# Kernel optimization log

Measured on AMD Instinct MI355X. Metric: run time of the kernel, lower is better.

The kernel has to match this reference:

```python
import jax, jax.numpy as jnp
import numpy as np

V = 23
C_IN = 256
C_OUT = 256
N = 16384
BN_EPS = 1e-5


def _make_shift(c, sign):
    # shift_in:  idx[i*c+j] = (i*c + j + j*c) % (c*V)
    # shift_out: idx[i*c+j] = (i*c + j - j*c) % (c*V)
    i = np.arange(V)[:, None]
    j = np.arange(c)[None, :]
    idx = (i * c + j + sign * j * c) % (c * V)
    return jnp.asarray(idx.reshape(-1), dtype=jnp.int32)


def setup_inputs() -> dict:
    key = jax.random.key(0)
    k1, k2, k3 = jax.random.split(key, 3)
    x0 = jax.random.normal(k1, (N, C_IN, V), dtype=jnp.float32)
    # Linear_weight ~ N(0, sqrt(1/out_channels))
    W = jax.random.normal(k2, (C_IN, C_OUT), dtype=jnp.float32) * np.sqrt(1.0 / C_OUT)
    bias = jnp.zeros((1, 1, C_OUT), dtype=jnp.float32)
    # Feature_Mask param (init 0 in original; randomized for a non-trivial baseline)
    mask = jax.random.normal(k3, (1, V, C_IN), dtype=jnp.float32) * 0.1
    bn_weight = jnp.ones((V * C_OUT,), dtype=jnp.float32)
    bn_bias = jnp.zeros((V * C_OUT,), dtype=jnp.float32)
    shift_in = _make_shift(C_IN, +1)
    shift_out = _make_shift(C_OUT, -1)
    return {"x0": x0, "W": W, "bias": bias, "mask": mask,
            "bn_weight": bn_weight, "bn_bias": bn_bias,
            "shift_in": shift_in, "shift_out": shift_out}


def reference(x0, W, bias, mask, bn_weight, bn_bias, shift_in, shift_out):
    n, c, v = x0.shape
    c_out = W.shape[1]
    # (n, c, v) -> (n, v*c), channel-shift gather
    x = jnp.transpose(x0, (0, 2, 1)).reshape(n, v * c)
    x = x[:, shift_in]                       # gather along feature dim
    x = x.reshape(n, v, c)
    x = x * (jnp.tanh(mask) + 1.0)           # learned soft mask
    x = jnp.einsum('nwc,cd->nwd', x, W) + bias
    x = x.reshape(n, v * c_out)
    x = x[:, shift_out]                      # shift-back gather
    # BatchNorm1d over v*c_out features, training-mode batch stats (biased var)
    mean = jnp.mean(x, axis=0)
    var = jnp.var(x, axis=0)
    x = (x - mean) * jax.lax.rsqrt(var + BN_EPS) * bn_weight + bn_bias
    x = x.reshape(n, v, c_out).transpose(0, 2, 1)
    # in_channels == out_channels -> down is identity
    x = x + x0
    return jax.nn.relu(x)
```

## Files before the change

kernel.cpp:

```cpp
#include <hip/hip_runtime.h>
#include <hip/hip_bf16.h>

#define NV 23
#define NTOT 16384
#define FLAT (NV * 256)
#define FLAT4 (FLAT / 4)
#define CH 184
#define NS 3
#define SLAB 23552

#define NB0 64
#define ROFF0 32768
#define NB1 64
#define ROFF1 32768
#define OOFF1 103424

#define NPART 256
#define WT8_OFF 248832
#define TAB8_OFF 314368
#define PSUM_OFF 337920
#define PSSQ_OFF (PSUM_OFF + NPART * FLAT * 4)
#define WS_NEED (PSSQ_OFF + NPART * FLAT * 4)

typedef short s16x8 __attribute__((ext_vector_type(8)));
typedef float f32x4 __attribute__((ext_vector_type(4)));
typedef unsigned u32x4 __attribute__((ext_vector_type(4)));
typedef long long i64t;

__device__ __forceinline__ int divNV(int x) { return (int)(((unsigned)x * 45591u) >> 20); }
__device__ __forceinline__ unsigned f2bf(float f) {
  unsigned u = __float_as_uint(f);
  u += 0x7fffu + ((u >> 16) & 1u);
  return u >> 16;
}
__device__ __forceinline__ int fsw(int w) { return ((w + (w >> 3)) * 3) & 7; }

__device__ __forceinline__ void gl_lds16(const void* g, void* l) {
  __builtin_amdgcn_global_load_lds(
      (const __attribute__((address_space(1))) unsigned*)(unsigned long long)(uintptr_t)g,
      (__attribute__((address_space(3))) unsigned*)(unsigned)(uintptr_t)l, 16, 0, 0);
}

__global__ void k_prep(const float* __restrict__ W, const float* __restrict__ mask,
                       short* __restrict__ Wt, char* __restrict__ Wt8,
                       unsigned* __restrict__ tab, unsigned* __restrict__ tab8,
                       float* __restrict__ sums) {
  int idx = blockIdx.x * 256 + threadIdx.x;
  int d = idx >> 8, c = idx & 255;
  float wv = W[c * 256 + d];
  Wt[idx] = (short)f2bf(wv);
  Wt8[idx] = (char)__builtin_amdgcn_cvt_pk_fp8_f32(wv, wv, 0, false);
  if (idx < FLAT) {
    int cc = divNV(idx);
    int v = idx - NV * cc;
    int cm = cc - NV * divNV(cc);
    int w = v - cm; w += (w >> 31) & NV;
    unsigned m2b = f2bf(tanhf(mask[(w << 8) + cc]) + 1.0f) << 16;
    tab[idx]  = m2b | (unsigned)((w << 9) + ((cc << 1) ^ (fsw(w) << 4)));
    tab8[idx] = m2b | (unsigned)((w << 8) + (cc ^ (fsw(w) << 4)));
  }
  if (idx < 2 * FLAT) sums[idx] = 0.0f;
}

__global__ void k_finalize(const float* __restrict__ sum, const float* __restrict__ ssq,
                           const float* __restrict__ psum, const float* __restrict__ pssq,
                           const float* __restrict__ bnw, const float* __restrict__ bnb,
                           float* __restrict__ An2, float* __restrict__ Bn2) {
  __shared__ float red[2][4][64];
  const int t = threadIdx.x;
  const int f0 = blockIdx.x * 64;
  if (psum) {
    const int fl = t & 63, c = t >> 6;
    float S = 0.f, Q = 0.f;
    for (int b = 0; b < 64; ++b) {
      S += psum[(size_t)(c * 64 + b) * FLAT + f0 + fl];
      Q += pssq[(size_t)(c * 64 + b) * FLAT + f0 + fl];
    }
    red[0][c][fl] = S;
    red[1][c][fl] = Q;
    __syncthreads();
  }
  if (t < 64) {
    int idx = f0 + t;
    float S, Q;
    if (psum) {
      S = red[0][0][t] + red[0][1][t] + red[0][2][t] + red[0][3][t];
      Q = red[1][0][t] + red[1][1][t] + red[1][2][t] + red[1][3][t];
    } else {
      S = sum[idx]; Q = ssq[idx];
    }
    int w = idx >> 8, d = idx & 255;
    float mean = S * (1.0f / NTOT);
    float var  = Q * (1.0f / NTOT) - mean * mean;
    float inv  = rsqrtf(var + 1e-5f);
    int i = w + d; i -= NV * divNV(i);
    float a = inv * bnw[i * 256 + d];
    An2[d * NV + i] = a;
    Bn2[d * NV + i] = bnb[i * 256 + d] - mean * a;
  }
}

__global__ __launch_bounds__(512) void k_stats(
    const float* __restrict__ x0, const char* __restrict__ Wt8,
    const unsigned* __restrict__ tab8, float* __restrict__ sum, float* __restrict__ ssq,
    float* __restrict__ psum, float* __restrict__ pssq) {
  __shared__ char smem[126976];

  const int tid = threadIdx.x;
  const int lane = tid & 63;
  const int wv = tid >> 6;
  const int l15 = lane & 15;
  const int lg = lane >> 4;
  const int d0 = wv * 32;
  const int ch0 = wv * CH;
  const int fr0 = fsw(l15) << 4;
  const int fr1 = fsw(16 + l15) << 4;

  i64t bfr8[2][8];
#pragma unroll
  for (int nt = 0; nt < 2; ++nt)
#pragma unroll
    for (int kt = 0; kt < 8; ++kt)
      bfr8[nt][kt] = *(const i64t*)(Wt8 + (d0 + nt * 16 + l15) * 256 + kt * 32 + lg * 8);

  u32x4 tbr[NS];
#pragma unroll
  for (int s = 0; s < NS; ++s)
    if (s * 64 + lane < CH) tbr[s] = *(const u32x4*)(tab8 + 4 * (ch0 + s * 64 + lane));

  for (int i = tid; i < 2304; i += 512) {
    int b = i / 576;
    *(int*)(smem + b * 8192 + 5888 + (i - b * 576) * 4) = 0;
  }

  float s1[2][2][4], s2[2][2][4];
#pragma unroll
  for (int mt = 0; mt < 2; ++mt)
#pragma unroll
    for (int nt = 0; nt < 2; ++nt)
#pragma unroll
      for (int r = 0; r < 4; ++r) { s1[mt][nt][r] = 0.f; s2[mt][nt][r] = 0.f; }

  const int nbase = blockIdx.x * NB0;

  auto stage = [&](int T) {
    if (T >= NB0) return;
    const char* gs = (const char*)(x0 + (size_t)(nbase + T) * FLAT);
    char* lb = smem + ROFF0 + (T % 4) * SLAB;
    gl_lds16(gs + (wv << 10) + lane * 16, lb + (wv << 10));
    gl_lds16(gs + ((8 + wv) << 10) + lane * 16, lb + ((8 + wv) << 10));
    if (wv < 7)
      gl_lds16(gs + ((16 + wv) << 10) + lane * 16, lb + ((16 + wv) << 10));
  };
  auto form = [&](int T) {
    if (T >= NB0) return;
    const char* rb = smem + ROFF0 + (T % 4) * SLAB;
    char* xb = smem + (T % 4) * 8192;
#pragma unroll
    for (int s = 0; s < NS; ++s)
      if (s * 64 + lane < CH) {
        f32x4 xv = *(const f32x4*)(rb + (ch0 + s * 64 + lane) * 16);
        u32x4 tb = tbr[s];
        float v0 = xv[0] * __uint_as_float(tb[0] & 0xffff0000u);
        float v1 = xv[1] * __uint_as_float(tb[1] & 0xffff0000u);
        float v2 = xv[2] * __uint_as_float(tb[2] & 0xffff0000u);
        float v3 = xv[3] * __uint_as_float(tb[3] & 0xffff0000u);
        int u01 = __builtin_amdgcn_cvt_pk_fp8_f32(v0, v1, 0, false);
        int u23 = __builtin_amdgcn_cvt_pk_fp8_f32(v2, v3, 0, false);
        xb[tb[0] & 0xffffu] = (char)u01;
        xb[tb[1] & 0xffffu] = (char)(u01 >> 8);
        xb[tb[2] & 0xffffu] = (char)u23;
        xb[tb[3] & 0xffffu] = (char)(u23 >> 8);
      }
  };
  auto mstep = [&](int T, f32x4 (*acc)[2]) {
    const char* xb = smem + (T % 4) * 8192;
    i64t a0[8], a1[8];
#pragma unroll
    for (int kt = 0; kt < 8; ++kt) {
      a0[kt] = *(const i64t*)(xb + (l15 << 8) + ((kt * 32 + lg * 8) ^ fr0));
      a1[kt] = *(const i64t*)(xb + ((16 + l15) << 8) + ((kt * 32 + lg * 8) ^ fr1));
    }
#pragma unroll
    for (int kt = 0; kt < 8; ++kt) {
#pragma unroll
      for (int nt = 0; nt < 2; ++nt) {
        acc[0][nt] = __builtin_amdgcn_mfma_f32_16x16x32_fp8_fp8(a0[kt], bfr8[nt][kt], acc[0][nt], 0, 0, 0);
        acc[1][nt] = __builtin_amdgcn_mfma_f32_16x16x32_fp8_fp8(a1[kt], bfr8[nt][kt], acc[1][nt], 0, 0, 0);
      }
    }
  };
  auto sstep = [&](f32x4 (*acc)[2]) {
#pragma unroll
    for (int mt = 0; mt < 2; ++mt)
#pragma unroll
      for (int nt = 0; nt < 2; ++nt)
#pragma unroll
        for (int r = 0; r < 4; ++r) {
          float y = acc[mt][nt][r];
          s1[mt][nt][r] += y;
          s2[mt][nt][r] += y * y;
        }
  };
  auto bar = []() {
    asm volatile("s_waitcnt lgkmcnt(0)" ::: "memory");
    __builtin_amdgcn_s_barrier();
    asm volatile("" ::: "memory");
  };

  stage(0); stage(1); stage(2); stage(3);
  asm volatile("s_waitcnt vmcnt(0)" ::: "memory");
  bar();
  form(0); form(1);
  for (int u = 0; u < NB0 / 2; ++u) {
    int t = 2 * u;
    asm volatile("s_waitcnt vmcnt(0)" ::: "memory");
    bar();
    stage(t + 4); stage(t + 5);
    form(t + 2); form(t + 3);
    f32x4 acc[2][2];
    __builtin_amdgcn_s_setprio(1);
#pragma unroll
    for (int mt = 0; mt < 2; ++mt)
#pragma unroll
      for (int nt = 0; nt < 2; ++nt) acc[mt][nt] = (f32x4){0.f, 0.f, 0.f, 0.f};
    mstep(t, acc);
    sstep(acc);
#pragma unroll
    for (int mt = 0; mt < 2; ++mt)
#pragma unroll
      for (int nt = 0; nt < 2; ++nt) acc[mt][nt] = (f32x4){0.f, 0.f, 0.f, 0.f};
    mstep(t + 1, acc);
    __builtin_amdgcn_s_setprio(0);
    sstep(acc);
  }
  if (psum) {
    float* ps = psum + (size_t)blockIdx.x * FLAT;
    float* pq = pssq + (size_t)blockIdx.x * FLAT;
#pragma unroll
    for (int mt = 0; mt < 2; ++mt)
#pragma unroll
      for (int nt = 0; nt < 2; ++nt)
#pragma unroll
        for (int r = 0; r < 4; ++r) {
          int w = mt * 16 + lg * 4 + r;
          if (w < NV) {
            int d = d0 + nt * 16 + l15;
            __builtin_nontemporal_store(s1[mt][nt][r], ps + (w << 8) + d);
            __builtin_nontemporal_store(s2[mt][nt][r], pq + (w << 8) + d);
          }
        }
  } else {
#pragma unroll
    for (int mt = 0; mt < 2; ++mt)
#pragma unroll
      for (int nt = 0; nt < 2; ++nt)
#pragma unroll
        for (int r = 0; r < 4; ++r) {
          int w = mt * 16 + lg * 4 + r;
          if (w < NV) {
            int d = d0 + nt * 16 + l15;
            atomicAdd(sum + (w << 8) + d, s1[mt][nt][r]);
            atomicAdd(ssq + (w << 8) + d, s2[mt][nt][r]);
          }
        }
  }
}

__global__ __launch_bounds__(512) void k_write(
    const float* __restrict__ x0, const short* __restrict__ Wt,
    const unsigned* __restrict__ tab,
    const float* __restrict__ An2, const float* __restrict__ Bn2,
    float* __restrict__ out) {
  __shared__ char smem[126976];
  float* O = (float*)(smem + OOFF1);

  const int tid = threadIdx.x;
  const int lane = tid & 63;
  const int wv = tid >> 6;
  const int l15 = lane & 15;
  const int lg = lane >> 4;
  const int d0 = wv * 32;
  const int ch0 = wv * CH;
  const int fr0 = fsw(l15) << 4;
  const int fr1 = fsw(16 + l15) << 4;

  s16x8 bfr[2][8];
#pragma unroll
  for (int nt = 0; nt < 2; ++nt)
#pragma unroll
    for (int kt = 0; kt < 8; ++kt)
      bfr[nt][kt] = *(const s16x8*)(Wt + (d0 + nt * 16 + l15) * 256 + kt * 32 + lg * 8);

  u32x4 tbr[NS];
#pragma unroll
  for (int s = 0; s < NS; ++s)
    if (s * 64 + lane < CH) tbr[s] = *(const u32x4*)(tab + 4 * (ch0 + s * 64 + lane));

  f32x4 anr[NS], bnr[NS];
#pragma unroll
  for (int s = 0; s < NS; ++s)
    if (s * 64 + lane < CH) {
      anr[s] = *(const f32x4*)(An2 + 4 * (ch0 + s * 64 + lane));
      bnr[s] = *(const f32x4*)(Bn2 + 4 * (ch0 + s * 64 + lane));
    }

  for (int i = tid; i < 2304; i += 512) {
    int b = i >= 1152;
    *(int*)(smem + b * 16384 + 11776 + (i - b * 1152) * 4) = 0;
  }

  const int nbase = blockIdx.x * NB1;
  auto nmap = [&](int T) { return nbase + (NB1 - 1 - T); };

  auto stage = [&](int T) {
    if (T >= NB1) return;
    const char* gs = (const char*)(x0 + (size_t)nmap(T) * FLAT);
    char* lb = smem + ROFF1 + (T % 3) * SLAB;
    gl_lds16(gs + (wv << 10) + lane * 16, lb + (wv << 10));
    gl_lds16(gs + ((8 + wv) << 10) + lane * 16, lb + ((8 + wv) << 10));
    if (wv < 7)
      gl_lds16(gs + ((16 + wv) << 10) + lane * 16, lb + ((16 + wv) << 10));
  };
  auto form = [&](int T) {
    if (T >= NB1) return;
    const char* rb = smem + ROFF1 + (T % 3) * SLAB;
    char* xb = smem + (T & 1) * 16384;
#pragma unroll
    for (int s = 0; s < NS; ++s)
      if (s * 64 + lane < CH) {
        f32x4 xv = *(const f32x4*)(rb + (ch0 + s * 64 + lane) * 16);
        u32x4 tb = tbr[s];
#pragma unroll
        for (int e = 0; e < 4; ++e) {
          unsigned tt = tb[e];
          *(short*)(xb + (tt & 0xffffu)) =
              (short)f2bf(xv[e] * __uint_as_float(tt & 0xffff0000u));
        }
      }
  };
  auto bar = []() {
    asm volatile("s_waitcnt lgkmcnt(0)" ::: "memory");
    __builtin_amdgcn_s_barrier();
    asm volatile("" ::: "memory");
  };

  stage(0); stage(1);
  asm volatile("s_waitcnt vmcnt(0)" ::: "memory");
  bar();
  form(0);

  for (int t = 0; t < NB1; ++t) {
    if (t) asm volatile("s_waitcnt vmcnt(3)" ::: "memory");
    else   asm volatile("s_waitcnt vmcnt(0)" ::: "memory");
    bar();
    stage(t + 2);
    form(t + 1);

    const char* xb = smem + (t & 1) * 16384;
    f32x4 acc[2][2];
#pragma unroll
    for (int mt = 0; mt < 2; ++mt)
#pragma unroll
      for (int nt = 0; nt < 2; ++nt) acc[mt][nt] = (f32x4){0.f, 0.f, 0.f, 0.f};
    __builtin_amdgcn_s_setprio(1);
#pragma unroll
    for (int kt = 0; kt < 8; ++kt) {
      s16x8 af[2];
      af[0] = *(const s16x8*)(xb + (l15 << 9) + ((kt * 64 + lg * 16) ^ fr0));
      af[1] = *(const s16x8*)(xb + ((16 + l15) << 9) + ((kt * 64 + lg * 16) ^ fr1));
#pragma unroll
      for (int mt = 0; mt < 2; ++mt)
#pragma unroll
        for (int nt = 0; nt < 2; ++nt)
          acc[mt][nt] = __builtin_amdgcn_mfma_f32_16x16x32_bf16(
              af[mt], bfr[nt][kt], acc[mt][nt], 0, 0, 0);
    }
    __builtin_amdgcn_s_setprio(0);

#pragma unroll
    for (int mt = 0; mt < 2; ++mt)
#pragma unroll
      for (int nt = 0; nt < 2; ++nt)
#pragma unroll
        for (int r = 0; r < 4; ++r) {
          int w = mt * 16 + lg * 4 + r;
          if (w < NV) {
            int d = d0 + nt * 16 + l15;
            int sj = w + d; sj -= NV * divNV(sj);
            O[d * NV + sj] = acc[mt][nt][r];
          }
        }
    const char* rb = smem + ROFF1 + (t % 3) * SLAB;
    float* og = out + (size_t)nmap(t) * FLAT;
#pragma unroll
    for (int s = 0; s < NS; ++s)
      if (s * 64 + lane < CH) {
        int i = ch0 + s * 64 + lane;
        f32x4 y = *(const f32x4*)(O + 4 * i);
        f32x4 sl = *(const f32x4*)(rb + i * 16);
        f32x4 o;
#pragma unroll
        for (int e = 0; e < 4; ++e)
          o[e] = fmaxf(fmaf(y[e], anr[s][e], bnr[s][e]) + sl[e], 0.0f);
        __builtin_nontemporal_store(o, (f32x4*)og + i);
      }
  }
}

extern "C" void kernel_launch(void* const* d_in, const int* in_sizes, int n_in,
                              void* d_out, int out_size, void* d_ws, size_t ws_size,
                              hipStream_t stream) {
  const float* x0   = (const float*)d_in[0];
  const float* W    = (const float*)d_in[1];
  const float* mask = (const float*)d_in[3];
  const float* bnw  = (const float*)d_in[4];
  const float* bnb  = (const float*)d_in[5];
  float* out = (float*)d_out;

  char* ws = (char*)d_ws;
  short* Wt      = (short*)ws;
  unsigned* tab  = (unsigned*)(ws + 131072);
  float* sum     = (float*)(ws + 154624);
  float* ssq     = (float*)(ws + 178176);
  float* An2     = (float*)(ws + 201728);
  float* Bn2     = (float*)(ws + 225280);
  char* Wt8      = ws + WT8_OFF;
  unsigned* tab8 = (unsigned*)(ws + TAB8_OFF);
  bool part = ws_size >= (size_t)WS_NEED;
  float* psum = part ? (float*)(ws + PSUM_OFF) : nullptr;
  float* pssq = part ? (float*)(ws + PSSQ_OFF) : nullptr;

  k_prep<<<256, 256, 0, stream>>>(W, mask, Wt, Wt8, tab, tab8, sum);
  k_stats<<<256, 512, 0, stream>>>(x0, Wt8, tab8, sum, ssq, psum, pssq);
  k_finalize<<<92, 256, 0, stream>>>(sum, ssq, psum, pssq, bnw, bnb, An2, Bn2);
  k_write<<<256, 512, 0, stream>>>(x0, Wt, tab, An2, Bn2, out);
}
```

Before: 249.5 us.

## Split stats kernel over twice the blocks with a shallower, smaller-LDS pipeline

The statistics kernel now launches 512 blocks, each handling 32 samples instead of 64. It replaces the four-slab, two-samples-per-step pipeline with two raw slabs and one sample per step, where each sample's form is done right after the previous sample's MFMA. This cuts LDS use from about 124 KB to about 78 KB, so two blocks can share a CU, giving more latency hiding and better load balance. In exchange there are twice as many per-block partial-sum buffers, so the finalize kernel reads more data, and the shorter lookahead leaves less prefetch depth.

```diff
diff --git a/kernel.cpp b/kernel.cpp
--- a/kernel.cpp
+++ b/kernel.cpp
@@ -9,13 +9,13 @@
 #define NS 3
 #define SLAB 23552
 
-#define NB0 64
+#define NB0 32
 #define ROFF0 32768
 #define NB1 64
 #define ROFF1 32768
 #define OOFF1 103424
 
-#define NPART 256
+#define NPART 512
 #define WT8_OFF 248832
 #define TAB8_OFF 314368
 #define PSUM_OFF 337920
@@ -72,9 +72,9 @@
   if (psum) {
     const int fl = t & 63, c = t >> 6;
     float S = 0.f, Q = 0.f;
-    for (int b = 0; b < 64; ++b) {
-      S += psum[(size_t)(c * 64 + b) * FLAT + f0 + fl];
-      Q += pssq[(size_t)(c * 64 + b) * FLAT + f0 + fl];
+    for (int b = 0; b < NPART / 4; ++b) {
+      S += psum[(size_t)(c * (NPART / 4) + b) * FLAT + f0 + fl];
+      Q += pssq[(size_t)(c * (NPART / 4) + b) * FLAT + f0 + fl];
     }
     red[0][c][fl] = S;
     red[1][c][fl] = Q;
@@ -104,7 +104,7 @@
     const float* __restrict__ x0, const char* __restrict__ Wt8,
     const unsigned* __restrict__ tab8, float* __restrict__ sum, float* __restrict__ ssq,
     float* __restrict__ psum, float* __restrict__ pssq) {
-  __shared__ char smem[126976];
+  __shared__ char smem[79872];
 
   const int tid = threadIdx.x;
   const int lane = tid & 63;
@@ -146,7 +146,7 @@
   auto stage = [&](int T) {
     if (T >= NB0) return;
     const char* gs = (const char*)(x0 + (size_t)(nbase + T) * FLAT);
-    char* lb = smem + ROFF0 + (T % 4) * SLAB;
+    char* lb = smem + ROFF0 + (T & 1) * SLAB;
     gl_lds16(gs + (wv << 10) + lane * 16, lb + (wv << 10));
     gl_lds16(gs + ((8 + wv) << 10) + lane * 16, lb + ((8 + wv) << 10));
     if (wv < 7)
@@ -154,7 +154,7 @@
   };
   auto form = [&](int T) {
     if (T >= NB0) return;
-    const char* rb = smem + ROFF0 + (T % 4) * SLAB;
+    const char* rb = smem + ROFF0 + (T & 1) * SLAB;
     char* xb = smem + (T % 4) * 8192;
 #pragma unroll
     for (int s = 0; s < NS; ++s)
@@ -190,7 +190,29 @@
       }
     }
   };
-  auto sstep = [&](f32x4 (*acc)[2]) {
+  auto bar = []() {
+    asm volatile("s_waitcnt lgkmcnt(0)" ::: "memory");
+    __builtin_amdgcn_s_barrier();
+    asm volatile("" ::: "memory");
+  };
+
+  stage(0); stage(1);
+  asm volatile("s_waitcnt vmcnt(0)" ::: "memory");
+  bar();
+  form(0);
+
+  for (int t = 0; t < NB0; ++t) {
+    asm volatile("s_waitcnt vmcnt(0)" ::: "memory");
+    bar();
+    stage(t + 2);
+    f32x4 acc[2][2];
+    __builtin_amdgcn_s_setprio(1);
+#pragma unroll
+    for (int mt = 0; mt < 2; ++mt)
+#pragma unroll
+      for (int nt = 0; nt < 2; ++nt) acc[mt][nt] = (f32x4){0.f, 0.f, 0.f, 0.f};
+    mstep(t, acc);
+    __builtin_amdgcn_s_setprio(0);
 #pragma unroll
     for (int mt = 0; mt < 2; ++mt)
 #pragma unroll
@@ -201,38 +223,7 @@
           s1[mt][nt][r] += y;
           s2[mt][nt][r] += y * y;
         }
-  };
-  auto bar = []() {
-    asm volatile("s_waitcnt lgkmcnt(0)" ::: "memory");
-    __builtin_amdgcn_s_barrier();
-    asm volatile("" ::: "memory");
-  };
-
-  stage(0); stage(1); stage(2); stage(3);
-  asm volatile("s_waitcnt vmcnt(0)" ::: "memory");
-  bar();
-  form(0); form(1);
-  for (int u = 0; u < NB0 / 2; ++u) {
-    int t = 2 * u;
-    asm volatile("s_waitcnt vmcnt(0)" ::: "memory");
-    bar();
-    stage(t + 4); stage(t + 5);
-    form(t + 2); form(t + 3);
-    f32x4 acc[2][2];
-    __builtin_amdgcn_s_setprio(1);
-#pragma unroll
-    for (int mt = 0; mt < 2; ++mt)
-#pragma unroll
-      for (int nt = 0; nt < 2; ++nt) acc[mt][nt] = (f32x4){0.f, 0.f, 0.f, 0.f};
-    mstep(t, acc);
-    sstep(acc);
-#pragma unroll
-    for (int mt = 0; mt < 2; ++mt)
-#pragma unroll
-      for (int nt = 0; nt < 2; ++nt) acc[mt][nt] = (f32x4){0.f, 0.f, 0.f, 0.f};
-    mstep(t + 1, acc);
-    __builtin_amdgcn_s_setprio(0);
-    sstep(acc);
+    form(t + 1);
   }
   if (psum) {
     float* ps = psum + (size_t)blockIdx.x * FLAT;
@@ -432,7 +423,7 @@
   float* pssq = part ? (float*)(ws + PSSQ_OFF) : nullptr;
 
   k_prep<<<256, 256, 0, stream>>>(W, mask, Wt, Wt8, tab, tab8, sum);
-  k_stats<<<256, 512, 0, stream>>>(x0, Wt8, tab8, sum, ssq, psum, pssq);
+  k_stats<<<512, 512, 0, stream>>>(x0, Wt8, tab8, sum, ssq, psum, pssq);
   k_finalize<<<92, 256, 0, stream>>>(sum, ssq, psum, pssq, bnw, bnb, An2, Bn2);
   k_write<<<256, 512, 0, stream>>>(x0, Wt, tab, An2, Bn2, out);
 }
```

After: 268.6 us. +7.6%, slower.

## Pack two samples per MFMA tile in stats pass to cut padded rows

Applied to the files above, without the earlier changes.

The stats kernel now places two batch samples (23 rows each) into one 48-row fp8 A tile, using a second gather table that offsets the second sample by 23 rows. Each pair then runs three 16-row MFMA groups instead of four mostly-padded ones, which removes wasted matrix work on zero-padded rows. Per-block partial sums grow to 46 rows and the finalize kernel folds the two halves back together. LDS layout and the zero-padding region change to match, and the finalize kernel reads twice as many partial values.

```diff
diff --git a/kernel.cpp b/kernel.cpp
--- a/kernel.cpp
+++ b/kernel.cpp
@@ -10,17 +10,19 @@
 #define SLAB 23552
 
 #define NB0 64
-#define ROFF0 32768
+#define ROFF0 24576
 #define NB1 64
 #define ROFF1 32768
 #define OOFF1 103424
 
 #define NPART 256
+#define PROWS 48
 #define WT8_OFF 248832
 #define TAB8_OFF 314368
-#define PSUM_OFF 337920
-#define PSSQ_OFF (PSUM_OFF + NPART * FLAT * 4)
-#define WS_NEED (PSSQ_OFF + NPART * FLAT * 4)
+#define TAB8B_OFF 337920
+#define PSUM_OFF 361472
+#define PSSQ_OFF (PSUM_OFF + NPART * PROWS * 256 * 4)
+#define WS_NEED (PSSQ_OFF + NPART * PROWS * 256 * 4)
 
 typedef short s16x8 __attribute__((ext_vector_type(8)));
 typedef float f32x4 __attribute__((ext_vector_type(4)));
@@ -44,7 +46,7 @@
 __global__ void k_prep(const float* __restrict__ W, const float* __restrict__ mask,
                        short* __restrict__ Wt, char* __restrict__ Wt8,
                        unsigned* __restrict__ tab, unsigned* __restrict__ tab8,
-                       float* __restrict__ sums) {
+                       unsigned* __restrict__ tab8b, float* __restrict__ sums) {
   int idx = blockIdx.x * 256 + threadIdx.x;
   int d = idx >> 8, c = idx & 255;
   float wv = W[c * 256 + d];
@@ -56,8 +58,9 @@
     int cm = cc - NV * divNV(cc);
     int w = v - cm; w += (w >> 31) & NV;
     unsigned m2b = f2bf(tanhf(mask[(w << 8) + cc]) + 1.0f) << 16;
-    tab[idx]  = m2b | (unsigned)((w << 9) + ((cc << 1) ^ (fsw(w) << 4)));
-    tab8[idx] = m2b | (unsigned)((w << 8) + (cc ^ (fsw(w) << 4)));
+    tab[idx]   = m2b | (unsigned)((w << 9) + ((cc << 1) ^ (fsw(w) << 4)));
+    tab8[idx]  = m2b | (unsigned)((w << 8) + (cc ^ (fsw(w) << 4)));
+    tab8b[idx] = m2b | (unsigned)(((w + NV) << 8) + (cc ^ (fsw(w + NV) << 4)));
   }
   if (idx < 2 * FLAT) sums[idx] = 0.0f;
 }
@@ -69,12 +72,17 @@
   __shared__ float red[2][4][64];
   const int t = threadIdx.x;
   const int f0 = blockIdx.x * 64;
+  const int wq = f0 >> 8;
+  const int dq = (f0 & 255);
   if (psum) {
     const int fl = t & 63, c = t >> 6;
+    size_t oA = (size_t)(wq << 8) + dq + fl;
+    size_t oB = (size_t)((wq + NV) << 8) + dq + fl;
     float S = 0.f, Q = 0.f;
     for (int b = 0; b < 64; ++b) {
-      S += psum[(size_t)(c * 64 + b) * FLAT + f0 + fl];
-      Q += pssq[(size_t)(c * 64 + b) * FLAT + f0 + fl];
+      size_t base = (size_t)(c * 64 + b) * (PROWS * 256);
+      S += psum[base + oA] + psum[base + oB];
+      Q += pssq[base + oA] + pssq[base + oB];
     }
     red[0][c][fl] = S;
     red[1][c][fl] = Q;
@@ -102,9 +110,10 @@
 
 __global__ __launch_bounds__(512) void k_stats(
     const float* __restrict__ x0, const char* __restrict__ Wt8,
-    const unsigned* __restrict__ tab8, float* __restrict__ sum, float* __restrict__ ssq,
+    const unsigned* __restrict__ tab8, const unsigned* __restrict__ tab8b,
+    float* __restrict__ sum, float* __restrict__ ssq,
     float* __restrict__ psum, float* __restrict__ pssq) {
-  __shared__ char smem[126976];
+  __shared__ char smem[118784];
 
   const int tid = threadIdx.x;
   const int lane = tid & 63;
@@ -115,6 +124,7 @@
   const int ch0 = wv * CH;
   const int fr0 = fsw(l15) << 4;
   const int fr1 = fsw(16 + l15) << 4;
+  const int fr2 = fsw(32 + l15) << 4;
 
   i64t bfr8[2][8];
 #pragma unroll
@@ -123,19 +133,22 @@
     for (int kt = 0; kt < 8; ++kt)
       bfr8[nt][kt] = *(const i64t*)(Wt8 + (d0 + nt * 16 + l15) * 256 + kt * 32 + lg * 8);
 
-  u32x4 tbr[NS];
+  u32x4 tbrA[NS], tbrB[NS];
 #pragma unroll
   for (int s = 0; s < NS; ++s)
-    if (s * 64 + lane < CH) tbr[s] = *(const u32x4*)(tab8 + 4 * (ch0 + s * 64 + lane));
-
-  for (int i = tid; i < 2304; i += 512) {
-    int b = i / 576;
-    *(int*)(smem + b * 8192 + 5888 + (i - b * 576) * 4) = 0;
-  }
-
-  float s1[2][2][4], s2[2][2][4];
-#pragma unroll
-  for (int mt = 0; mt < 2; ++mt)
+    if (s * 64 + lane < CH) {
+      tbrA[s] = *(const u32x4*)(tab8 + 4 * (ch0 + s * 64 + lane));
+      tbrB[s] = *(const u32x4*)(tab8b + 4 * (ch0 + s * 64 + lane));
+    }
+
+  if (tid < 256) {
+    int b = tid >> 7;
+    *(int*)(smem + b * 12288 + 11776 + (tid & 127) * 4) = 0;
+  }
+
+  float s1[3][2][4], s2[3][2][4];
+#pragma unroll
+  for (int mt = 0; mt < 3; ++mt)
 #pragma unroll
     for (int nt = 0; nt < 2; ++nt)
 #pragma unroll
@@ -152,47 +165,76 @@
     if (wv < 7)
       gl_lds16(gs + ((16 + wv) << 10) + lane * 16, lb + ((16 + wv) << 10));
   };
-  auto form = [&](int T) {
-    if (T >= NB0) return;
-    const char* rb = smem + ROFF0 + (T % 4) * SLAB;
-    char* xb = smem + (T % 4) * 8192;
+  auto formpair = [&](int P) {
+    if (2 * P >= NB0) return;
+    const char* ra = smem + ROFF0 + ((2 * P) % 4) * SLAB;
+    const char* rb = smem + ROFF0 + ((2 * P + 1) % 4) * SLAB;
+    char* xb = smem + (P & 1) * 12288;
 #pragma unroll
     for (int s = 0; s < NS; ++s)
       if (s * 64 + lane < CH) {
+        f32x4 xa = *(const f32x4*)(ra + (ch0 + s * 64 + lane) * 16);
         f32x4 xv = *(const f32x4*)(rb + (ch0 + s * 64 + lane) * 16);
-        u32x4 tb = tbr[s];
-        float v0 = xv[0] * __uint_as_float(tb[0] & 0xffff0000u);
-        float v1 = xv[1] * __uint_as_float(tb[1] & 0xffff0000u);
-        float v2 = xv[2] * __uint_as_float(tb[2] & 0xffff0000u);
-        float v3 = xv[3] * __uint_as_float(tb[3] & 0xffff0000u);
-        int u01 = __builtin_amdgcn_cvt_pk_fp8_f32(v0, v1, 0, false);
-        int u23 = __builtin_amdgcn_cvt_pk_fp8_f32(v2, v3, 0, false);
-        xb[tb[0] & 0xffffu] = (char)u01;
-        xb[tb[1] & 0xffffu] = (char)(u01 >> 8);
-        xb[tb[2] & 0xffffu] = (char)u23;
-        xb[tb[3] & 0xffffu] = (char)(u23 >> 8);
+        u32x4 ta = tbrA[s], tb = tbrB[s];
+#pragma unroll
+        for (int e = 0; e < 4; e += 2) {
+          float a0 = xa[e] * __uint_as_float(ta[e] & 0xffff0000u);
+          float a1 = xa[e + 1] * __uint_as_float(ta[e + 1] & 0xffff0000u);
+          float b0 = xv[e] * __uint_as_float(tb[e] & 0xffff0000u);
+          float b1 = xv[e + 1] * __uint_as_float(tb[e + 1] & 0xffff0000u);
+          int ua = __builtin_amdgcn_cvt_pk_fp8_f32(a0, a1, 0, false);
+          int ub = __builtin_amdgcn_cvt_pk_fp8_f32(b0, b1, 0, false);
+          xb[ta[e] & 0xffffu] = (char)ua;
+          xb[ta[e + 1] & 0xffffu] = (char)(ua >> 8);
+          xb[tb[e] & 0xffffu] = (char)ub;
+          xb[tb[e + 1] & 0xffffu] = (char)(ub >> 8);
+        }
       }
   };
-  auto mstep = [&](int T, f32x4 (*acc)[2]) {
-    const char* xb = smem + (T % 4) * 8192;
-    i64t a0[8], a1[8];
-#pragma unroll
-    for (int kt = 0; kt < 8; ++kt) {
-      a0[kt] = *(const i64t*)(xb + (l15 << 8) + ((kt * 32 + lg * 8) ^ fr0));
-      a1[kt] = *(const i64t*)(xb + ((16 + l15) << 8) + ((kt * 32 + lg * 8) ^ fr1));
-    }
-#pragma unroll
-    for (int kt = 0; kt < 8; ++kt) {
-#pragma unroll
-      for (int nt = 0; nt < 2; ++nt) {
-        acc[0][nt] = __builtin_amdgcn_mfma_f32_16x16x32_fp8_fp8(a0[kt], bfr8[nt][kt], acc[0][nt], 0, 0, 0);
-        acc[1][nt] = __builtin_amdgcn_mfma_f32_16x16x32_fp8_fp8(a1[kt], bfr8[nt][kt], acc[1][nt], 0, 0, 0);
-      }
-    }
-  };
-  auto sstep = [&](f32x4 (*acc)[2]) {
-#pragma unroll
-    for (int mt = 0; mt < 2; ++mt)
+  auto mstep = [&](int P, f32x4 (*acc)[2]) {
+    const char* xb = smem + (P & 1) * 12288;
+#pragma unroll
+    for (int mt = 0; mt < 3; ++mt) {
+      const int row = mt * 16 + l15;
+      const int fr = mt == 0 ? fr0 : (mt == 1 ? fr1 : fr2);
+      i64t a[8];
+#pragma unroll
+      for (int kt = 0; kt < 8; ++kt)
+        a[kt] = *(const i64t*)(xb + (row << 8) + ((kt * 32 + lg * 8) ^ fr));
+#pragma unroll
+      for (int kt = 0; kt < 8; ++kt)
+#pragma unroll
+        for (int nt = 0; nt < 2; ++nt)
+          acc[mt][nt] = __builtin_amdgcn_mfma_f32_16x16x32_fp8_fp8(
+              a[kt], bfr8[nt][kt], acc[mt][nt], 0, 0, 0);
+    }
+  };
+  auto bar = []() {
+    asm volatile("s_waitcnt lgkmcnt(0)" ::: "memory");
+    __builtin_amdgcn_s_barrier();
+    asm volatile("" ::: "memory");
+  };
+
+  stage(0); stage(1); stage(2); stage(3);
+  asm volatile("s_waitcnt vmcnt(0)" ::: "memory");
+  bar();
+  formpair(0);
+
+  for (int u = 0; u < NB0 / 2; ++u) {
+    asm volatile("s_waitcnt vmcnt(0)" ::: "memory");
+    bar();
+    stage(2 * u + 4); stage(2 * u + 5);
+    formpair(u + 1);
+    f32x4 acc[3][2];
+    __builtin_amdgcn_s_setprio(1);
+#pragma unroll
+    for (int mt = 0; mt < 3; ++mt)
+#pragma unroll
+      for (int nt = 0; nt < 2; ++nt) acc[mt][nt] = (f32x4){0.f, 0.f, 0.f, 0.f};
+    mstep(u, acc);
+    __builtin_amdgcn_s_setprio(0);
+#pragma unroll
+    for (int mt = 0; mt < 3; ++mt)
 #pragma unroll
       for (int nt = 0; nt < 2; ++nt)
 #pragma unroll
@@ -201,64 +243,34 @@
           s1[mt][nt][r] += y;
           s2[mt][nt][r] += y * y;
         }
-  };
-  auto bar = []() {
-    asm volatile("s_waitcnt lgkmcnt(0)" ::: "memory");
-    __builtin_amdgcn_s_barrier();
-    asm volatile("" ::: "memory");
-  };
-
-  stage(0); stage(1); stage(2); stage(3);
-  asm volatile("s_waitcnt vmcnt(0)" ::: "memory");
-  bar();
-  form(0); form(1);
-  for (int u = 0; u < NB0 / 2; ++u) {
-    int t = 2 * u;
-    asm volatile("s_waitcnt vmcnt(0)" ::: "memory");
-    bar();
-    stage(t + 4); stage(t + 5);
-    form(t + 2); form(t + 3);
-    f32x4 acc[2][2];
-    __builtin_amdgcn_s_setprio(1);
-#pragma unroll
-    for (int mt = 0; mt < 2; ++mt)
-#pragma unroll
-      for (int nt = 0; nt < 2; ++nt) acc[mt][nt] = (f32x4){0.f, 0.f, 0.f, 0.f};
-    mstep(t, acc);
-    sstep(acc);
-#pragma unroll
-    for (int mt = 0; mt < 2; ++mt)
-#pragma unroll
-      for (int nt = 0; nt < 2; ++nt) acc[mt][nt] = (f32x4){0.f, 0.f, 0.f, 0.f};
-    mstep(t + 1, acc);
-    __builtin_amdgcn_s_setprio(0);
-    sstep(acc);
-  }
+  }
+
   if (psum) {
-    float* ps = psum + (size_t)blockIdx.x * FLAT;
-    float* pq = pssq + (size_t)blockIdx.x * FLAT;
-#pragma unroll
-    for (int mt = 0; mt < 2; ++mt)
+    float* ps = psum + (size_t)blockIdx.x * (PROWS * 256);
+    float* pq = pssq + (size_t)blockIdx.x * (PROWS * 256);
+#pragma unroll
+    for (int mt = 0; mt < 3; ++mt)
 #pragma unroll
       for (int nt = 0; nt < 2; ++nt)
 #pragma unroll
         for (int r = 0; r < 4; ++r) {
-          int w = mt * 16 + lg * 4 + r;
-          if (w < NV) {
+          int row = mt * 16 + lg * 4 + r;
+          if (row < 46) {
             int d = d0 + nt * 16 + l15;
-            __builtin_nontemporal_store(s1[mt][nt][r], ps + (w << 8) + d);
-            __builtin_nontemporal_store(s2[mt][nt][r], pq + (w << 8) + d);
+            __builtin_nontemporal_store(s1[mt][nt][r], ps + (row << 8) + d);
+            __builtin_nontemporal_store(s2[mt][nt][r], pq + (row << 8) + d);
           }
         }
   } else {
 #pragma unroll
-    for (int mt = 0; mt < 2; ++mt)
+    for (int mt = 0; mt < 3; ++mt)
 #pragma unroll
       for (int nt = 0; nt < 2; ++nt)
 #pragma unroll
         for (int r = 0; r < 4; ++r) {
-          int w = mt * 16 + lg * 4 + r;
-          if (w < NV) {
+          int row = mt * 16 + lg * 4 + r;
+          if (row < 46) {
+            int w = row - (row >= NV ? NV : 0);
             int d = d0 + nt * 16 + l15;
             atomicAdd(sum + (w << 8) + d, s1[mt][nt][r]);
             atomicAdd(ssq + (w << 8) + d, s2[mt][nt][r]);
@@ -419,20 +431,21 @@
   float* out = (float*)d_out;
 
   char* ws = (char*)d_ws;
-  short* Wt      = (short*)ws;
-  unsigned* tab  = (unsigned*)(ws + 131072);
-  float* sum     = (float*)(ws + 154624);
-  float* ssq     = (float*)(ws + 178176);
-  float* An2     = (float*)(ws + 201728);
-  float* Bn2     = (float*)(ws + 225280);
-  char* Wt8      = ws + WT8_OFF;
-  unsigned* tab8 = (unsigned*)(ws + TAB8_OFF);
+  short* Wt       = (short*)ws;
+  unsigned* tab   = (unsigned*)(ws + 131072);
+  float* sum      = (float*)(ws + 154624);
+  float* ssq      = (float*)(ws + 178176);
+  float* An2      = (float*)(ws + 201728);
+  float* Bn2      = (float*)(ws + 225280);
+  char* Wt8       = ws + WT8_OFF;
+  unsigned* tab8  = (unsigned*)(ws + TAB8_OFF);
+  unsigned* tab8b = (unsigned*)(ws + TAB8B_OFF);
   bool part = ws_size >= (size_t)WS_NEED;
   float* psum = part ? (float*)(ws + PSUM_OFF) : nullptr;
   float* pssq = part ? (float*)(ws + PSSQ_OFF) : nullptr;
 
-  k_prep<<<256, 256, 0, stream>>>(W, mask, Wt, Wt8, tab, tab8, sum);
-  k_stats<<<256, 512, 0, stream>>>(x0, Wt8, tab8, sum, ssq, psum, pssq);
+  k_prep<<<256, 256, 0, stream>>>(W, mask, Wt, Wt8, tab, tab8, tab8b, sum);
+  k_stats<<<256, 512, 0, stream>>>(x0, Wt8, tab8, tab8b, sum, ssq, psum, pssq);
   k_finalize<<<92, 256, 0, stream>>>(sum, ssq, psum, pssq, bnw, bnb, An2, Bn2);
   k_write<<<256, 512, 0, stream>>>(x0, Wt, tab, An2, Bn2, out);
 }
```

Result: faster. 241.2 us (-3.3%).
